# Optimization experiments

Measured on AMD Instinct MI355X. Metric: run time of the kernel, lower is better.

## Reference

```python
import jax, jax.numpy as jnp
import numpy as np

B, CIN, COUT, H, W, WDIM = 16, 256, 256, 64, 64, 512


def setup_inputs() -> dict:
    key = jax.random.key(0)
    ks = jax.random.split(key, 4)
    return {
        "x": jax.random.normal(ks[0], (B, CIN, H, W), dtype=jnp.float32),
        "w": jax.random.normal(ks[1], (B, WDIM), dtype=jnp.float32),
        "affine_w": jax.random.normal(ks[2], (CIN, WDIM), dtype=jnp.float32),
        "affine_b": jnp.ones((CIN,), dtype=jnp.float32),
        "weight": jax.random.normal(ks[3], (COUT, CIN, 1, 1), dtype=jnp.float32),
        "bias": jnp.zeros((COUT,), dtype=jnp.float32),
    }


def reference(x, w, affine_w, affine_b, weight, bias):
    # Affine: FullyConnectedLayer with weight_gain = 1/sqrt(w_dim), bias_init=1
    wg = 1.0 / np.sqrt(WDIM).astype(np.float32)
    styles = w @ (affine_w.T * wg) + affine_b  # [B, CIN]

    # Pre-normalize weight and styles (demodulate branch)
    wk = weight[:, :, 0, 0]  # [COUT, CIN] (1x1 kernel)
    wk = wk * jax.lax.rsqrt(jnp.mean(jnp.square(weight), axis=(1, 2, 3)))[:, None]
    s = styles * jax.lax.rsqrt(jnp.mean(jnp.square(styles)))  # [B, CIN]

    # Per-sample modulated weights: [B, COUT, CIN]
    wb = wk[None, :, :] * s[:, None, :]
    dcoef = jax.lax.rsqrt(jnp.sum(jnp.square(wb), axis=2) + 1e-8)  # [B, COUT]
    wb = wb * dcoef[:, :, None]

    # Grouped 1x1 conv == batched GEMM over spatial positions
    y = jnp.einsum('bihw,boi->bohw', x, wb) + bias[None, :, None, None]

    # Bilinear upsample x2 (align_corners=False == half-pixel, jax default)
    y = jax.image.resize(y, (B, COUT, 2 * H, 2 * W), method='bilinear')
    return y
```

## Files before the change

### kernel.cpp

```cpp
#include <hip/hip_runtime.h>
#include <hip/hip_bf16.h>

#define B_   16
#define CIN  256
#define COUT 256
#define HH   64
#define WW   64
#define WDIM 512
#define OH   128
#define OW   128

typedef __attribute__((ext_vector_type(8))) short short8;
typedef __attribute__((ext_vector_type(4))) float f32x4;

__device__ __forceinline__ unsigned short f2bf(float f) {
    __hip_bfloat16 h = __float2bfloat16(f);
    return *reinterpret_cast<unsigned short*>(&h);
}
__device__ __forceinline__ float bf2f(unsigned short u) {
    unsigned int t = ((unsigned int)u) << 16;
    return *reinterpret_cast<float*>(&t);
}


__global__ __launch_bounds__(256) void k_styles(const float* __restrict__ w,
                                                const float* __restrict__ aw,
                                                const float* __restrict__ ab,
                                                float* __restrict__ ws) {
    int b = blockIdx.x, i = threadIdx.x;
    const float4* wr = (const float4*)(w + b * WDIM);
    const float4* ar = (const float4*)(aw + (size_t)i * WDIM);
    float acc = 0.f;
    #pragma unroll 4
    for (int k = 0; k < WDIM / 4; ++k) {
        float4 wv = wr[k], av = ar[k];
        acc += wv.x * av.x + wv.y * av.y + wv.z * av.z + wv.w * av.w;
    }
    const float wg = 0.04419417382415922f;
    float st = acc * wg + ab[i];
    ws[64 + b * CIN + i] = st;
    __shared__ float sred[256];
    sred[i] = st * st;
    __syncthreads();
    for (int s = 128; s > 0; s >>= 1) {
        if (i < s) sred[i] += sred[i + s];
        __syncthreads();
    }
    if (i == 0) ws[b] = sred[0];
}

__global__ __launch_bounds__(64) void k_wb(const float* __restrict__ weight,
                                           const float* __restrict__ ws,
                                           unsigned short* __restrict__ wb) {
    int o = blockIdx.x, b = blockIdx.y, l = threadIdx.x;
    float tot = 0.f;
    #pragma unroll
    for (int j = 0; j < B_; ++j) tot += ws[j];
    float srs = rsqrtf(tot / (float)(B_ * CIN));
    float4 wk = *(const float4*)(weight + (size_t)o * CIN + l * 4);
    float ss = wk.x * wk.x + wk.y * wk.y + wk.z * wk.z + wk.w * wk.w;
    #pragma unroll
    for (int off = 32; off; off >>= 1) ss += __shfl_xor(ss, off);
    float wkn = rsqrtf(ss / (float)CIN);
    float4 st = *(const float4*)(ws + 64 + b * CIN + l * 4);
    float4 t;
    t.x = wk.x * wkn * st.x * srs;
    t.y = wk.y * wkn * st.y * srs;
    t.z = wk.z * wkn * st.z * srs;
    t.w = wk.w * wkn * st.w * srs;
    float s2 = t.x * t.x + t.y * t.y + t.z * t.z + t.w * t.w;
    #pragma unroll
    for (int off = 32; off; off >>= 1) s2 += __shfl_xor(s2, off);
    float dcoef = rsqrtf(s2 + 1e-8f);
    ushort4 pk;
    pk.x = f2bf(t.x * dcoef);
    pk.y = f2bf(t.y * dcoef);
    pk.z = f2bf(t.z * dcoef);
    pk.w = f2bf(t.w * dcoef);
    *(ushort4*)(wb + ((size_t)b * COUT + o) * CIN + l * 4) = pk;
}

__global__ __launch_bounds__(512, 2) void k_fused(const float* __restrict__ x,
                                                  const float* __restrict__ bias,
                                                  const unsigned short* __restrict__ wb,
                                                  float* __restrict__ out) {
    __shared__ __align__(16) unsigned short xt[128 * CIN];
    __shared__ __align__(16) unsigned int yl[COUT * 64];
    const int r = blockIdx.x;
    const int b = blockIdx.y;
    const int tid = threadIdx.x;
    const int lane = tid & 63;
    const int wv = tid >> 6;
    const int lo = lane & 15, hi = lane >> 4;

    const unsigned short* wbb = wb + (size_t)b * COUT * CIN;
    const int m0_0 = (wv * 2 + 0) * 16;
    const int m0_1 = (wv * 2 + 1) * 16;
    short8 breg0[8], breg1[8];
    {
        const unsigned short* wrow = wbb + (size_t)(m0_0 + lo) * CIN + hi * 8;
        #pragma unroll
        for (int ks = 0; ks < 8; ++ks) breg0[ks] = *(const short8*)(wrow + ks * 32);
    }

    {
        const int c4 = tid & 15;
        const int rowsel = (tid >> 4) & 1;
        const int ig = tid >> 5;
        const int grow = min(r + rowsel, HH - 1);
        const float* xp = x + (size_t)b * CIN * (HH * WW) + (size_t)grow * WW + c4 * 4;
        const int pxbase = rowsel * 64 + c4 * 4;
        #pragma unroll
        for (int p = 0; p < 8; ++p) {
            const int i0 = ig * 16 + p * 2;
            float4 v0 = *(const float4*)(xp + (size_t)i0 * (HH * WW));
            float4 v1 = *(const float4*)(xp + (size_t)(i0 + 1) * (HH * WW));
            const int ib = i0 >> 3, e = i0 & 7;
            #pragma unroll
            for (int j = 0; j < 4; ++j) {
                const int px = pxbase + j;
                float f0 = (j == 0) ? v0.x : (j == 1) ? v0.y : (j == 2) ? v0.z : v0.w;
                float f1 = (j == 0) ? v1.x : (j == 1) ? v1.y : (j == 2) ? v1.z : v1.w;
                unsigned int pk = (unsigned int)f2bf(f0) | ((unsigned int)f2bf(f1) << 16);
                const int swz = ib ^ (px & 31) ^ ((px >> 2) & 7);
                *(unsigned int*)&xt[px * 256 + (swz << 3) + e] = pk;
            }
        }
    }
    __syncthreads();

    {
        const unsigned short* wrow = wbb + (size_t)(m0_1 + lo) * CIN + hi * 8;
        #pragma unroll
        for (int ks = 0; ks < 8; ++ks) breg1[ks] = *(const short8*)(wrow + ks * 32);
    }

    #pragma unroll
    for (int c = 0; c < 2; ++c) {
        const int m0 = c ? m0_1 : m0_0;
        const int o = m0 + lo;
        const float bs = bias[o];
        const int rot = 2 * (o & 15);
        unsigned int* yrow = &yl[o * 64];
        #pragma unroll
        for (int g = 0; g < 8; ++g) {
            f32x4 acc = {0.f, 0.f, 0.f, 0.f};
            #pragma unroll
            for (int ks = 0; ks < 8; ++ks) {
                const int px = g * 16 + lo;
                const int ib = ks * 4 + hi;
                const int swz = ib ^ (px & 31) ^ ((px >> 2) & 7);
                short8 a = *(const short8*)&xt[px * 256 + (swz << 3)];
                acc = __builtin_amdgcn_mfma_f32_16x16x32_bf16(
                        a, c ? breg1[ks] : breg0[ks], acc, 0, 0, 0);
            }
            const int p2 = g * 8 + hi * 2;
            unsigned int u0 = (unsigned int)f2bf(acc[0] + bs) | ((unsigned int)f2bf(acc[1] + bs) << 16);
            unsigned int u1 = (unsigned int)f2bf(acc[2] + bs) | ((unsigned int)f2bf(acc[3] + bs) << 16);
            const int cc = (p2 + rot) & 63;
            yrow[cc] = u0;
            yrow[cc + 1] = u1;
        }
    }
    __syncthreads();

    const int ostart = (r == 0) ? 0 : (2 * r + 1);
    const int nrows = (r == 0) ? 3 : ((r == HH - 1) ? 1 : 2);
    const int iters = nrows * 16;
    const int h = tid >> 5;
    const int t = tid & 31;

    for (int i = 0; i < iters; ++i) {
        const int task = i * 16 + h;
        const int o = task & 255;
        const int ori = task >> 8;
        const int orow = ostart + ori;
        const int yr0 = (orow - 1) >> 1;
        const int lr0 = min(max(yr0, 0), HH - 1) - r;
        const int lr1 = min(yr0 + 1, HH - 1) - r;
        const float wr0 = (orow & 1) ? 0.75f : 0.25f;
        const float wr1 = 1.f - wr0;
        const int rot = 2 * (o & 15);
        const unsigned int* yrow = &yl[o * 64];
        unsigned int M0 = yrow[(lr0 * 32 + t + rot) & 63];
        unsigned int M1 = yrow[(lr1 * 32 + t + rot) & 63];
        float mB = bf2f((unsigned short)(M0 & 0xffff)), mC = bf2f((unsigned short)(M0 >> 16));
        float nB = bf2f((unsigned short)(M1 & 0xffff)), nC = bf2f((unsigned short)(M1 >> 16));
        float vB = wr0 * mB + wr1 * nB;
        float vC = wr0 * mC + wr1 * nC;
        float vA = __shfl_up(vC, 1, 32);   if (t == 0)  vA = vB;
        float vD = __shfl_down(vB, 1, 32); if (t == 31) vD = vC;
        float4 ov;
        ov.x = 0.25f * vA + 0.75f * vB;
        ov.y = 0.75f * vB + 0.25f * vC;
        ov.z = 0.25f * vB + 0.75f * vC;
        ov.w = 0.75f * vC + 0.25f * vD;
        float* op = out + (((size_t)(b * COUT + o) * OH) + orow) * OW + 4 * t;
        *(float4*)op = ov;
    }
}

extern "C" void kernel_launch(void* const* d_in, const int* in_sizes, int n_in,
                              void* d_out, int out_size, void* d_ws, size_t ws_size,
                              hipStream_t stream) {
    (void)in_sizes; (void)n_in; (void)out_size; (void)ws_size;
    const float* x      = (const float*)d_in[0];
    const float* w      = (const float*)d_in[1];
    const float* aw     = (const float*)d_in[2];
    const float* ab     = (const float*)d_in[3];
    const float* weight = (const float*)d_in[4];
    const float* bias   = (const float*)d_in[5];
    float* out = (float*)d_out;
    float* wsf = (float*)d_ws;
    unsigned short* wb = (unsigned short*)((char*)d_ws + 32768);

    hipLaunchKernelGGL(k_styles, dim3(16), dim3(256), 0, stream, w, aw, ab, wsf);
    hipLaunchKernelGGL(k_wb, dim3(COUT, B_), dim3(64), 0, stream, weight, wsf, wb);
    hipLaunchKernelGGL(k_fused, dim3(HH, B_), dim3(512), 0, stream, x, bias, wb, out);
}
```

Baseline: 120.4 us.

## Alias x-tile and y-tile shared memory to raise occupancy in fused kernel

The xt and yl shared buffers (64KB each) now alias one 64KB region. All MFMA work finishes into registers (acc0/acc1) before a barrier, and only then is the bf16 output tile written over the input tile. Launch bounds go from 2 to 4 blocks per CU, and the B fragments are loaded in two phases through one register array to save VGPRs. This halves LDS per block so more blocks can be resident, at the cost of an extra barrier and 64 accumulator registers held live.

```diff
diff --git a/kernel.cpp b/kernel.cpp
--- a/kernel.cpp
+++ b/kernel.cpp
@@ -80,12 +80,14 @@
     *(ushort4*)(wb + ((size_t)b * COUT + o) * CIN + l * 4) = pk;
 }
 
-__global__ __launch_bounds__(512, 2) void k_fused(const float* __restrict__ x,
-                                                  const float* __restrict__ bias,
-                                                  const unsigned short* __restrict__ wb,
-                                                  float* __restrict__ out) {
-    __shared__ __align__(16) unsigned short xt[128 * CIN];
-    __shared__ __align__(16) unsigned int yl[COUT * 64];
+__global__ __launch_bounds__(512, 4) void k_fused3(const float* __restrict__ x,
+                                                   const float* __restrict__ bias,
+                                                   const unsigned short* __restrict__ wb,
+                                                   float* __restrict__ out) {
+    __shared__ __align__(16) unsigned char smem[65536];
+    unsigned short* xt = (unsigned short*)smem;
+    unsigned int*  yl = (unsigned int*)smem;
+
     const int r = blockIdx.x;
     const int b = blockIdx.y;
     const int tid = threadIdx.x;
@@ -94,13 +96,14 @@
     const int lo = lane & 15, hi = lane >> 4;
 
     const unsigned short* wbb = wb + (size_t)b * COUT * CIN;
-    const int m0_0 = (wv * 2 + 0) * 16;
-    const int m0_1 = (wv * 2 + 1) * 16;
-    short8 breg0[8], breg1[8];
+    const int m0_0 = wv * 32;
+    const int m0_1 = wv * 32 + 16;
+
+    short8 breg[8];
     {
-        const unsigned short* wrow = wbb + (size_t)(m0_0 + lo) * CIN + hi * 8;
-        #pragma unroll
-        for (int ks = 0; ks < 8; ++ks) breg0[ks] = *(const short8*)(wrow + ks * 32);
+        const unsigned short* wr0 = wbb + (size_t)(m0_0 + lo) * CIN + hi * 8;
+        #pragma unroll
+        for (int ks = 0; ks < 8; ++ks) breg[ks] = *(const short8*)(wr0 + ks * 32);
     }
 
     {
@@ -129,11 +132,39 @@
     }
     __syncthreads();
 
+    f32x4 acc0[8], acc1[8];
+    #pragma unroll
+    for (int g = 0; g < 8; ++g) {
+        f32x4 a4 = {0.f, 0.f, 0.f, 0.f};
+        #pragma unroll
+        for (int ks = 0; ks < 8; ++ks) {
+            const int px = g * 16 + lo;
+            const int ib = ks * 4 + hi;
+            const int swz = ib ^ (px & 31) ^ ((px >> 2) & 7);
+            short8 a = *(const short8*)&xt[px * 256 + (swz << 3)];
+            a4 = __builtin_amdgcn_mfma_f32_16x16x32_bf16(a, breg[ks], a4, 0, 0, 0);
+        }
+        acc0[g] = a4;
+    }
     {
-        const unsigned short* wrow = wbb + (size_t)(m0_1 + lo) * CIN + hi * 8;
-        #pragma unroll
-        for (int ks = 0; ks < 8; ++ks) breg1[ks] = *(const short8*)(wrow + ks * 32);
-    }
+        const unsigned short* wr1 = wbb + (size_t)(m0_1 + lo) * CIN + hi * 8;
+        #pragma unroll
+        for (int ks = 0; ks < 8; ++ks) breg[ks] = *(const short8*)(wr1 + ks * 32);
+    }
+    #pragma unroll
+    for (int g = 0; g < 8; ++g) {
+        f32x4 a4 = {0.f, 0.f, 0.f, 0.f};
+        #pragma unroll
+        for (int ks = 0; ks < 8; ++ks) {
+            const int px = g * 16 + lo;
+            const int ib = ks * 4 + hi;
+            const int swz = ib ^ (px & 31) ^ ((px >> 2) & 7);
+            short8 a = *(const short8*)&xt[px * 256 + (swz << 3)];
+            a4 = __builtin_amdgcn_mfma_f32_16x16x32_bf16(a, breg[ks], a4, 0, 0, 0);
+        }
+        acc1[g] = a4;
+    }
+    __syncthreads();
 
     #pragma unroll
     for (int c = 0; c < 2; ++c) {
@@ -144,19 +175,10 @@
         unsigned int* yrow = &yl[o * 64];
         #pragma unroll
         for (int g = 0; g < 8; ++g) {
-            f32x4 acc = {0.f, 0.f, 0.f, 0.f};
-            #pragma unroll
-            for (int ks = 0; ks < 8; ++ks) {
-                const int px = g * 16 + lo;
-                const int ib = ks * 4 + hi;
-                const int swz = ib ^ (px & 31) ^ ((px >> 2) & 7);
-                short8 a = *(const short8*)&xt[px * 256 + (swz << 3)];
-                acc = __builtin_amdgcn_mfma_f32_16x16x32_bf16(
-                        a, c ? breg1[ks] : breg0[ks], acc, 0, 0, 0);
-            }
+            f32x4 a4 = c ? acc1[g] : acc0[g];
             const int p2 = g * 8 + hi * 2;
-            unsigned int u0 = (unsigned int)f2bf(acc[0] + bs) | ((unsigned int)f2bf(acc[1] + bs) << 16);
-            unsigned int u1 = (unsigned int)f2bf(acc[2] + bs) | ((unsigned int)f2bf(acc[3] + bs) << 16);
+            unsigned int u0 = (unsigned int)f2bf(a4[0] + bs) | ((unsigned int)f2bf(a4[1] + bs) << 16);
+            unsigned int u1 = (unsigned int)f2bf(a4[2] + bs) | ((unsigned int)f2bf(a4[3] + bs) << 16);
             const int cc = (p2 + rot) & 63;
             yrow[cc] = u0;
             yrow[cc + 1] = u1;
@@ -216,5 +238,5 @@
 
     hipLaunchKernelGGL(k_styles, dim3(16), dim3(256), 0, stream, w, aw, ab, wsf);
     hipLaunchKernelGGL(k_wb, dim3(COUT, B_), dim3(64), 0, stream, weight, wsf, wb);
-    hipLaunchKernelGGL(k_fused, dim3(HH, B_), dim3(512), 0, stream, x, bias, wb, out);
-}
+    hipLaunchKernelGGL(k_fused3, dim3(HH, B_), dim3(512), 0, stream, x, bias, wb, out);
+}
```

Result: slower. 208.7 us (+73.4%).
